# Optimization experiments

Measured on AMD Instinct MI355X. Metric: run time of the kernel, lower is better.

## Reference

```python
import jax, jax.numpy as jnp
import numpy as np
import math

L, B, D, H = 2048, 4, 1024, 16
DK = D // H
DFF = 4 * D
EPS = 1e-5


def setup_inputs() -> dict:
    key = jax.random.key(0)
    ks = jax.random.split(key, 16)
    s = 1.0 / math.sqrt(D)
    sf = 1.0 / math.sqrt(DFF)
    return {
        "x": jax.random.normal(ks[0], (L, B, D), jnp.float32),
        "Wq": jax.random.normal(ks[1], (D, D), jnp.float32) * s,
        "bq": jnp.zeros((D,), jnp.float32),
        "Wk": jax.random.normal(ks[2], (D, D), jnp.float32) * s,
        "bk": jnp.zeros((D,), jnp.float32),
        "Wv": jax.random.normal(ks[3], (D, D), jnp.float32) * s,
        "bv": jnp.zeros((D,), jnp.float32),
        "Wo": jax.random.normal(ks[4], (D, D), jnp.float32) * s,
        "bo": jnp.zeros((D,), jnp.float32),
        "W1": jax.random.normal(ks[5], (D, DFF), jnp.float32) * s,
        "b1": jnp.zeros((DFF,), jnp.float32),
        "W2": jax.random.normal(ks[6], (DFF, D), jnp.float32) * sf,
        "b2": jnp.zeros((D,), jnp.float32),
        "g1": jnp.ones((D,), jnp.float32),
        "be1": jnp.zeros((D,), jnp.float32),
        "g2": jnp.ones((D,), jnp.float32),
        "be2": jnp.zeros((D,), jnp.float32),
    }


def _layer_norm(x, g, b):
    mu = jnp.mean(x, axis=-1, keepdims=True)
    var = jnp.var(x, axis=-1, keepdims=True)
    return (x - mu) * jax.lax.rsqrt(var + EPS) * g + b


def reference(x, Wq, bq, Wk, bk, Wv, bv, Wo, bo, W1, b1, W2, b2, g1, be1, g2, be2):
    # x: (L, B, D)
    q = x @ Wq + bq
    k = x @ Wk + bk
    v = x @ Wv + bv
    # (L,B,H,dk) -> (B,H,L,dk)
    q = q.reshape(L, B, H, DK).transpose(1, 2, 0, 3)
    k = k.reshape(L, B, H, DK).transpose(1, 2, 0, 3)
    v = v.reshape(L, B, H, DK).transpose(1, 2, 0, 3)
    scale = 1.0 / math.sqrt(DK)
    scores = jnp.einsum('bhqd,bhkd->bhqk', q, k) * scale
    w = jax.nn.softmax(scores, axis=-1)
    attn = jnp.einsum('bhqk,bhkd->bhqd', w, v)  # (B,H,L,dk)
    attn = attn.transpose(2, 0, 1, 3).reshape(L, B, D)
    attn_out = attn @ Wo + bo
    x = _layer_norm(x + attn_out, g1, be1)
    h = jax.nn.gelu(x @ W1 + b1, approximate=False)
    ff = h @ W2 + b2
    return _layer_norm(x + ff, g2, be2)
```

## Files before the change

### kernel.cpp

```cpp
#include <hip/hip_runtime.h>

#define L_   2048
#define B_   4
#define D_   1024
#define H_   16
#define DK_  64
#define DFF_ 4096
#define NT_  (L_*B_)

typedef unsigned short u16;
typedef unsigned int   u32;
typedef __bf16 bf16x8 __attribute__((ext_vector_type(8)));
typedef float  f32x4  __attribute__((ext_vector_type(4)));

__device__ __forceinline__ u16 f2bf(float f) {
  u32 u = __float_as_uint(f);
  u += 0x7fffu + ((u >> 16) & 1u);
  return (u16)(u >> 16);
}
__device__ __forceinline__ float bf2f(u32 lo16) {
  return __uint_as_float(lo16 << 16);
}

#define GLDS16(g, l) __builtin_amdgcn_global_load_lds( \
    (const __attribute__((address_space(1))) void*)(g), \
    (__attribute__((address_space(3))) void*)(l), 16, 0, 0)

#define SCQ_ 0.18033688011112042f

__global__ __launch_bounds__(256) void transpose_w_k(
    const float* __restrict__ W, u16* __restrict__ Wt, int K, int N)
{
  __shared__ float tile[32][33];
  int n0 = blockIdx.x * 32, k0 = blockIdx.y * 32;
  int tx = threadIdx.x, ty = threadIdx.y;
#pragma unroll
  for (int i = ty; i < 32; i += 8)
    tile[i][tx] = W[(size_t)(k0 + i) * N + n0 + tx];
  __syncthreads();
#pragma unroll
  for (int i = ty; i < 32; i += 8)
    Wt[(size_t)(n0 + i) * K + k0 + tx] = f2bf(tile[tx][i]);
}

__global__ __launch_bounds__(256) void transpose_w4_k(
    const float* __restrict__ W0, const float* __restrict__ W1,
    const float* __restrict__ W2, const float* __restrict__ W3,
    u16* __restrict__ dst)
{
  __shared__ float tile[32][33];
  int z = blockIdx.z;
  const float* W = (z == 0) ? W0 : (z == 1) ? W1 : (z == 2) ? W2 : W3;
  u16* Wt = dst + (size_t)z * 1048576;
  int n0 = blockIdx.x * 32, k0 = blockIdx.y * 32;
  int tx = threadIdx.x, ty = threadIdx.y;
#pragma unroll
  for (int i = ty; i < 32; i += 8)
    tile[i][tx] = W[(size_t)(k0 + i) * 1024 + n0 + tx];
  __syncthreads();
#pragma unroll
  for (int i = ty; i < 32; i += 8)
    Wt[(size_t)(n0 + i) * 1024 + k0 + tx] = f2bf(tile[tx][i]);
}

__global__ __launch_bounds__(256) void f32_to_bf16_k(
    const float* __restrict__ in, u16* __restrict__ out, int n4)
{
  int i = blockIdx.x * 256 + threadIdx.x;
  if (i >= n4) return;
  float4 v = ((const float4*)in)[i];
  uint2 r;
  r.x = (u32)f2bf(v.x) | ((u32)f2bf(v.y) << 16);
  r.y = (u32)f2bf(v.z) | ((u32)f2bf(v.w) << 16);
  ((uint2*)out)[i] = r;
}

__global__ __launch_bounds__(256) void bias_concat_k(
    const float* __restrict__ bq, const float* __restrict__ bk,
    const float* __restrict__ bv, float* __restrict__ o)
{
  int i = blockIdx.x * 256 + threadIdx.x;
  float v = (i < 1024) ? bq[i] : ((i < 2048) ? bk[i - 1024] : bv[i - 2048]);
  o[i] = v;
}

template<int BN, int EPI>
__global__ __launch_bounds__(512, 2)
void gemm_pipe(const u16* __restrict__ A, const u16* __restrict__ Bt,
               const float* __restrict__ bias, const void* __restrict__ res,
               u16* __restrict__ outb, int M, int N, int K)
{
  constexpr int BM = 256;
  constexpr int NI  = 2 + BN / 128;
  constexpr int NWN = BN / 64;
  constexpr int NWM = 8 / NWN;
  constexpr int MIT = (BM / NWM) / 16;
  constexpr int NPH = MIT / 4;
  constexpr int BUFB = (BM + BN) * 64;
  __shared__ char SM[4 * BUFB];

  const int tid = threadIdx.x;
  const int w = tid >> 6, lane = tid & 63;
  const int l15 = lane & 15, l4 = lane >> 4;
  const int NK = K >> 5;

  const int gx = gridDim.x;
  int nwg = gx * gridDim.y;
  int id = blockIdx.y * gx + blockIdx.x;
  int q = nwg >> 3, r = nwg & 7;
  int xcd = id & 7, idx = id >> 3;
  int wg = (xcd < r ? xcd * (q + 1) : r * (q + 1) + (xcd - r) * q) + idx;
  const int m0 = (wg / gx) * BM, n0 = (wg % gx) * BN;
  const int wm = (w / NWN) * (BM / NWM), wn = (w % NWN) * 64;

  const u16* gsrc[NI];
#pragma unroll
  for (int k = 0; k < NI; ++k) {
    int o = k * 8192 + tid * 16;
    int col8 = (((o >> 4) ^ (o >> 6)) & 3);
    if (o < BM * 64) {
      int rrow = o >> 6;
      gsrc[k] = A + (size_t)(m0 + rrow) * K + col8 * 8;
    } else {
      int br = (o - BM * 64) >> 6;
      gsrc[k] = Bt + (size_t)(n0 + br) * K + col8 * 8;
    }
  }

  auto stage = [&](int t3, int k) {
    const u16* s = (t3 < NK) ? gsrc[k] + (size_t)t3 * 32 : gsrc[k];
    GLDS16(s, SM + (t3 & 3) * BUFB + k * 8192 + w * 1024);
  };

  for (int t3 = 0; t3 < 3; ++t3)
#pragma unroll
    for (int k = 0; k < NI; ++k) stage(t3, k);
  if constexpr (BN == 256) asm volatile("s_waitcnt vmcnt(8)" ::: "memory");
  else                     asm volatile("s_waitcnt vmcnt(6)" ::: "memory");
  asm volatile("s_barrier" ::: "memory");

  f32x4 acc[MIT][4];
#pragma unroll
  for (int i = 0; i < MIT; ++i)
#pragma unroll
    for (int j = 0; j < 4; ++j) acc[i][j] = (f32x4){0.f, 0.f, 0.f, 0.f};

  const int csw = (l4 ^ (l15 & 3)) * 16;

  for (int t = 0; t < NK; ++t) {
    const char* rb = SM + (t & 3) * BUFB;
    bf16x8 bfr[4];
#pragma unroll
    for (int ph = 0; ph < NPH; ++ph) {
      bf16x8 af[4];
#pragma unroll
      for (int mi = 0; mi < 4; ++mi)
        af[mi] = *(const bf16x8*)(rb + (wm + ph * 64 + mi * 16 + l15) * 64 + csw);
      if (ph == 0) {
#pragma unroll
        for (int nj = 0; nj < 4; ++nj)
          bfr[nj] = *(const bf16x8*)(rb + BM * 64 + (wn + nj * 16 + l15) * 64 + csw);
      }
      if constexpr (NPH == 2) {
        stage(t + 3, ph * 2 + 0);
        stage(t + 3, ph * 2 + 1);
      } else {
        stage(t + 3, 0); stage(t + 3, 1); stage(t + 3, 2);
      }
      asm volatile("s_barrier" ::: "memory");
      __builtin_amdgcn_s_setprio(1);
#pragma unroll
      for (int mi = 0; mi < 4; ++mi)
#pragma unroll
        for (int nj = 0; nj < 4; ++nj)
          acc[ph * 4 + mi][nj] = __builtin_amdgcn_mfma_f32_16x16x32_bf16(
              af[mi], bfr[nj], acc[ph * 4 + mi][nj], 0, 0, 0);
      __builtin_amdgcn_s_setprio(0);
      if (ph == NPH - 1) {
        if constexpr (BN == 256) asm volatile("s_waitcnt vmcnt(8)" ::: "memory");
        else                     asm volatile("s_waitcnt vmcnt(6)" ::: "memory");
      }
      asm volatile("s_barrier" ::: "memory");
    }
  }
  asm volatile("s_waitcnt vmcnt(0)" ::: "memory");

  const int gm = m0 + wm + l4 * 4;
  const int gn = n0 + wn + l15;
#pragma unroll
  for (int mi = 0; mi < MIT; ++mi) {
#pragma unroll
    for (int nj = 0; nj < 4; ++nj) {
      int col = gn + nj * 16;
      float bv = bias[col];
#pragma unroll
      for (int rr = 0; rr < 4; ++rr) {
        int row = gm + mi * 16 + rr;
        float v = acc[mi][nj][rr] + bv;
        if (EPI == 2) {
          float gv = 0.5f * v * (1.f + erff(v * 0.70710678118654752f));
          outb[(size_t)row * N + col] = f2bf(gv);
        } else if (EPI == 3) {
          int which = col >> 10, c1 = col & 1023;
          int ll = row >> 2, bb = row & 3;
          int hh = c1 >> 6, dd = c1 & 63;
          if (which == 0) v *= SCQ_;
          outb[(size_t)which * 8388608 +
               ((((size_t)(bb * H_ + hh)) * L_ + ll) << 6) + dd] = f2bf(v);
        } else if (EPI == 5) {
          size_t idxo = (size_t)row * N + col;
          outb[idxo] = f2bf(v + ((const float*)res)[idxo]);
        } else {
          size_t idxo = (size_t)row * N + col;
          outb[idxo] = f2bf(v + bf2f(((const u16*)res)[idxo]));
        }
      }
    }
  }
}

__global__ __launch_bounds__(256, 3)
void attn_fwd2(const u16* __restrict__ qp, const u16* __restrict__ kp,
               const u16* __restrict__ vp, u16* __restrict__ op)
{
  __shared__ u16 Ks[64 * 64];
  __shared__ u16 Vt[64 * 64];
  const int tid = threadIdx.x, w = tid >> 6, lane = tid & 63;
  const int l15 = lane & 15, l4 = lane >> 4;
  const int n = blockIdx.x;
  const int bh = (n & 7) | ((n >> 7) << 3);
  const int qi = (n >> 3) & 15;
  const int q0 = qi * 128;
  const u16* qb = qp + (size_t)bh * L_ * DK_;
  const u16* kb = kp + (size_t)bh * L_ * DK_;
  const u16* vb = vp + (size_t)bh * L_ * DK_;

  bf16x8 qf[2][2];
#pragma unroll
  for (int g = 0; g < 2; ++g)
#pragma unroll
    for (int kk = 0; kk < 2; ++kk)
      qf[g][kk] = *(const bf16x8*)&qb[(size_t)(q0 + g * 64 + w * 16 + l15) * DK_ +
                                      kk * 32 + l4 * 8];

  f32x4 accO[2][4];
#pragma unroll
  for (int g = 0; g < 2; ++g)
#pragma unroll
    for (int i = 0; i < 4; ++i) accO[g][i] = (f32x4){0.f, 0.f, 0.f, 0.f};
  float mrun[2] = {-1e30f, -1e30f}, lsum[2] = {0.f, 0.f};

  int rho0 = tid >> 3, rho1 = (256 + tid) >> 3, cseg = lane & 7;
  int kv0 = (rho0 & 32) | ((rho0 & 12) << 1) | ((rho0 & 16) >> 2) | (rho0 & 3);
  int kv1 = (rho1 & 32) | ((rho1 & 12) << 1) | ((rho1 & 16) >> 2) | (rho1 & 3);
  const u16* ksrc0 = kb + (size_t)kv0 * DK_ + ((cseg ^ (rho0 & 7)) << 3);
  const u16* ksrc1 = kb + (size_t)kv1 * DK_ + ((cseg ^ (rho1 & 7)) << 3);
  u16* kdst0 = &Ks[(w * 64) * 8];
  u16* kdst1 = &Ks[(256 + w * 64) * 8];

  const int vseg = tid & 7, vkvp = tid >> 3;
  const u16* vsrc = vb + (size_t)(vkvp * 2) * DK_ + vseg * 8;
  u32* vdst[8];
#pragma unroll
  for (int dd2 = 0; dd2 < 4; ++dd2) {
    int d0 = vseg * 8 + dd2 * 2, d1 = d0 + 1;
    vdst[dd2 * 2] = (u32*)((char*)Vt + d0 * 128 +
        ((((vkvp >> 2) ^ (d0 & 7) ^ (d0 >> 3)) << 4) | ((vkvp & 3) << 2)));
    vdst[dd2 * 2 + 1] = (u32*)((char*)Vt + d1 * 128 +
        ((((vkvp >> 2) ^ (d1 & 7) ^ (d1 >> 3)) << 4) | ((vkvp & 3) << 2)));
  }

  auto softmax_pack = [&](f32x4 (&s)[4], float& mr, float& ls,
                          f32x4 (&aO)[4], u32 (&pk)[2][4]) {
    float pm = fmaxf(fmaxf(s[0][0], s[0][1]), s[0][2]);
    pm = fmaxf(fmaxf(pm, s[0][3]), s[1][0]);
    pm = fmaxf(fmaxf(pm, s[1][1]), s[1][2]);
    pm = fmaxf(fmaxf(pm, s[1][3]), s[2][0]);
    pm = fmaxf(fmaxf(pm, s[2][1]), s[2][2]);
    pm = fmaxf(fmaxf(pm, s[2][3]), s[3][0]);
    pm = fmaxf(fmaxf(pm, s[3][1]), s[3][2]);
    pm = fmaxf(pm, s[3][3]);
    pm = fmaxf(pm, __shfl_xor(pm, 16));
    pm = fmaxf(pm, __shfl_xor(pm, 32));
    if (!__all(pm - mr <= 8.f)) {
      float mn = fmaxf(mr, pm);
      float alpha = exp2f(mr - mn);
      mr = mn;
      ls *= alpha;
#pragma unroll
      for (int rr = 0; rr < 4; ++rr) {
        float a4 = __shfl(alpha, l4 * 4 + rr);
        aO[0][rr] *= a4; aO[1][rr] *= a4; aO[2][rr] *= a4; aO[3][rr] *= a4;
      }
    }
#pragma unroll
    for (int i = 0; i < 4; ++i)
#pragma unroll
      for (int rr = 0; rr < 4; ++rr) s[i][rr] = exp2f(s[i][rr] - mr);
    float ps = 0.f;
#pragma unroll
    for (int i = 0; i < 4; ++i)
      ps += (s[i][0] + s[i][1]) + (s[i][2] + s[i][3]);
    ps += __shfl_xor(ps, 16);
    ps += __shfl_xor(ps, 32);
    ls += ps;
#pragma unroll
    for (int kk = 0; kk < 2; ++kk)
#pragma unroll
      for (int j2 = 0; j2 < 4; ++j2) {
        int nb = kk * 2 + (j2 >> 1);
        int rr = (j2 & 1) * 2;
        u32 rres;
        asm("v_cvt_pk_bf16_f32 %0, %1, %2" : "=v"(rres)
            : "v"(s[nb][rr]), "v"(s[nb][rr + 1]));
        pk[kk][j2] = rres;
      }
  };

  for (int t0 = 0; t0 < L_; t0 += 64) {
    __syncthreads();
    GLDS16(ksrc0 + (size_t)t0 * DK_, kdst0);
    GLDS16(ksrc1 + (size_t)t0 * DK_, kdst1);
    {
      const u16* src = vsrc + (size_t)t0 * DK_;
      uint4 a = *(const uint4*)src;
      uint4 b = *(const uint4*)(src + DK_);
#pragma unroll
      for (int dd2 = 0; dd2 < 4; ++dd2) {
        u32 ai = ((const u32*)&a)[dd2], bi = ((const u32*)&b)[dd2];
        *vdst[dd2 * 2]     = __builtin_amdgcn_perm(bi, ai, 0x05040100u);
        *vdst[dd2 * 2 + 1] = __builtin_amdgcn_perm(bi, ai, 0x07060302u);
      }
    }
    __syncthreads();

    f32x4 s0[4], s1[4];
#pragma unroll
    for (int i = 0; i < 4; ++i) {
      s0[i] = (f32x4){0.f, 0.f, 0.f, 0.f};
      s1[i] = (f32x4){0.f, 0.f, 0.f, 0.f};
    }
#pragma unroll
    for (int kk = 0; kk < 2; ++kk) {
#pragma unroll
      for (int nb = 0; nb < 4; ++nb) {
        int row = nb * 16 + l15;
        bf16x8 kf = *(const bf16x8*)((const char*)Ks + row * 128 +
                                     (((kk * 4 + l4) ^ (row & 7)) << 4));
        s0[nb] = __builtin_amdgcn_mfma_f32_16x16x32_bf16(kf, qf[0][kk], s0[nb], 0, 0, 0);
        s1[nb] = __builtin_amdgcn_mfma_f32_16x16x32_bf16(kf, qf[1][kk], s1[nb], 0, 0, 0);
      }
    }

    u32 pk0[2][4], pk1[2][4];
    softmax_pack(s0, mrun[0], lsum[0], accO[0], pk0);
    softmax_pack(s1, mrun[1], lsum[1], accO[1], pk1);

#pragma unroll
    for (int kk = 0; kk < 2; ++kk) {
      bf16x8 pa0, pa1;
      ((u32*)&pa0)[0] = pk0[kk][0]; ((u32*)&pa0)[1] = pk0[kk][1];
      ((u32*)&pa0)[2] = pk0[kk][2]; ((u32*)&pa0)[3] = pk0[kk][3];
      ((u32*)&pa1)[0] = pk1[kk][0]; ((u32*)&pa1)[1] = pk1[kk][1];
      ((u32*)&pa1)[2] = pk1[kk][2]; ((u32*)&pa1)[3] = pk1[kk][3];
#pragma unroll
      for (int nb2 = 0; nb2 < 4; ++nb2) {
        int drow = nb2 * 16 + l15;
        bf16x8 vf = *(const bf16x8*)((const char*)Vt + drow * 128 +
                                     (((kk * 4 + l4) ^ (drow & 7) ^ (drow >> 3)) << 4));
        accO[0][nb2] = __builtin_amdgcn_mfma_f32_16x16x32_bf16(pa0, vf, accO[0][nb2], 0, 0, 0);
        accO[1][nb2] = __builtin_amdgcn_mfma_f32_16x16x32_bf16(pa1, vf, accO[1][nb2], 0, 0, 0);
      }
    }
  }

  const int bb = bh >> 4, hh = bh & 15;
#pragma unroll
  for (int g = 0; g < 2; ++g) {
    float invl = 1.f / lsum[g];
#pragma unroll
    for (int rr = 0; rr < 4; ++rr) {
      float rl = __shfl(invl, l4 * 4 + rr);
      int qg = q0 + g * 64 + w * 16 + l4 * 4 + rr;
      size_t base = ((size_t)qg * B_ + bb) * D_ + hh * 64;
#pragma unroll
      for (int nb2 = 0; nb2 < 4; ++nb2)
        op[base + nb2 * 16 + l15] = f2bf(accO[g][nb2][rr] * rl);
    }
  }
}

__global__ __launch_bounds__(256) void layernorm_bf_k(
    const u16* __restrict__ y, const float* __restrict__ g, const float* __restrict__ be,
    float* __restrict__ of, u16* __restrict__ ob)
{
  int row = blockIdx.x, tid = threadIdx.x;
  uint2 raw = *(const uint2*)&y[(size_t)row * D_ + tid * 4];
  float v0 = bf2f(raw.x & 0xffffu), v1 = bf2f(raw.x >> 16);
  float v2 = bf2f(raw.y & 0xffffu), v3 = bf2f(raw.y >> 16);
  float s = (v0 + v1) + (v2 + v3);
  float ss = v0 * v0 + v1 * v1 + v2 * v2 + v3 * v3;
#pragma unroll
  for (int msk = 32; msk >= 1; msk >>= 1) {
    s += __shfl_xor(s, msk);
    ss += __shfl_xor(ss, msk);
  }
  __shared__ float rs[4], rss[4];
  if ((tid & 63) == 0) { rs[tid >> 6] = s; rss[tid >> 6] = ss; }
  __syncthreads();
  s = rs[0] + rs[1] + rs[2] + rs[3];
  ss = rss[0] + rss[1] + rss[2] + rss[3];
  float mu = s * (1.f / D_);
  float var = ss * (1.f / D_) - mu * mu;
  float rstd = rsqrtf(var + 1e-5f);
  int c = tid * 4;
  float o0 = (v0 - mu) * rstd * g[c + 0] + be[c + 0];
  float o1 = (v1 - mu) * rstd * g[c + 1] + be[c + 1];
  float o2 = (v2 - mu) * rstd * g[c + 2] + be[c + 2];
  float o3 = (v3 - mu) * rstd * g[c + 3] + be[c + 3];
  if (of) {
    float4 o = {o0, o1, o2, o3};
    *(float4*)&of[(size_t)row * D_ + c] = o;
  }
  if (ob) {
    uint2 r;
    r.x = (u32)f2bf(o0) | ((u32)f2bf(o1) << 16);
    r.y = (u32)f2bf(o2) | ((u32)f2bf(o3) << 16);
    *(uint2*)&ob[(size_t)row * D_ + c] = r;
  }
}

extern "C" void kernel_launch(void* const* d_in, const int* in_sizes, int n_in,
                              void* d_out, int out_size, void* d_ws, size_t ws_size,
                              hipStream_t stream)
{
  const float* x   = (const float*)d_in[0];
  const float* Wq  = (const float*)d_in[1];
  const float* bq  = (const float*)d_in[2];
  const float* Wk  = (const float*)d_in[3];
  const float* bk  = (const float*)d_in[4];
  const float* Wv  = (const float*)d_in[5];
  const float* bv  = (const float*)d_in[6];
  const float* Wo  = (const float*)d_in[7];
  const float* bo  = (const float*)d_in[8];
  const float* W1f = (const float*)d_in[9];
  const float* b1  = (const float*)d_in[10];
  const float* W2f = (const float*)d_in[11];
  const float* b2  = (const float*)d_in[12];
  const float* g1  = (const float*)d_in[13];
  const float* be1 = (const float*)d_in[14];
  const float* g2  = (const float*)d_in[15];
  const float* be2 = (const float*)d_in[16];

  char* ws = (char*)d_ws;
  const size_t MB = 1024 * 1024;
  u16* WqT  = (u16*)(ws + 0 * MB);
  u16* WoT  = (u16*)(ws + 6 * MB);
  u16* W1T  = (u16*)(ws + 8 * MB);
  u16* W2T  = (u16*)(ws + 16 * MB);
  u16* xb   = (u16*)(ws + 24 * MB);
  u16* qp   = (u16*)(ws + 40 * MB);
  u16* astd = (u16*)(ws + 88 * MB);
  u16* yb   = (u16*)(ws + 104 * MB);
  u16* x1b  = (u16*)(ws + 120 * MB);
  u16* hbuf = (u16*)(ws + 136 * MB);
  float* bcat = (float*)(ws + 200 * MB);
  u16* kp = qp + 8388608;
  u16* vp = qp + 16777216;

  dim3 tb(32, 8);
  transpose_w4_k<<<dim3(32, 32, 4), tb, 0, stream>>>(Wq, Wk, Wv, Wo, WqT);
  transpose_w_k<<<dim3(128, 32), tb, 0, stream>>>(W1f, W1T, D_, DFF_);
  transpose_w_k<<<dim3(32, 128), tb, 0, stream>>>(W2f, W2T, DFF_, D_);
  f32_to_bf16_k<<<NT_ * D_ / 4 / 256, 256, 0, stream>>>(x, xb, NT_ * D_ / 4);
  bias_concat_k<<<12, 256, 0, stream>>>(bq, bk, bv, bcat);

  gemm_pipe<128, 3><<<dim3(24, 32), 512, 0, stream>>>(
      xb, WqT, bcat, nullptr, qp, NT_, 3072, D_);

  attn_fwd2<<<1024, 256, 0, stream>>>(qp, kp, vp, astd);

  gemm_pipe<128, 5><<<dim3(8, 32), 512, 0, stream>>>(
      astd, WoT, bo, x, yb, NT_, D_, D_);
  layernorm_bf_k<<<NT_, 256, 0, stream>>>(yb, g1, be1, nullptr, x1b);
  gemm_pipe<256, 2><<<dim3(16, 32), 512, 0, stream>>>(
      x1b, W1T, b1, nullptr, hbuf, NT_, DFF_, D_);
  gemm_pipe<128, 6><<<dim3(8, 32), 512, 0, stream>>>(
      hbuf, W2T, b2, x1b, yb, NT_, D_, DFF_);
  layernorm_bf_k<<<NT_, 256, 0, stream>>>(yb, g2, be2, (float*)d_out, nullptr);
}
```

Measured before the change: 494.4 us.

## Double-buffer K/V tiles in attention kernel to overlap loads with MFMA

Attention kernel now keeps two LDS buffers for K and transposed V and prefetches the next tile (K via global-to-LDS loads, V via register loads packed into LDS after softmax) while computing on the current one. This drops one of the two barriers per iteration and hides global load latency behind compute. LDS use doubles to 32KB per block, which may reduce occupancy at launch bound 3 blocks/CU.

```diff
diff --git a/kernel.cpp b/kernel.cpp
--- a/kernel.cpp
+++ b/kernel.cpp
@@ -223,8 +223,8 @@
 void attn_fwd2(const u16* __restrict__ qp, const u16* __restrict__ kp,
                const u16* __restrict__ vp, u16* __restrict__ op)
 {
-  __shared__ u16 Ks[64 * 64];
-  __shared__ u16 Vt[64 * 64];
+  __shared__ u16 Ks[2][64 * 64];
+  __shared__ u16 Vt[2][64 * 64];
   const int tid = threadIdx.x, w = tid >> 6, lane = tid & 63;
   const int l15 = lane & 15, l4 = lane >> 4;
   const int n = blockIdx.x;
@@ -255,20 +255,27 @@
   int kv1 = (rho1 & 32) | ((rho1 & 12) << 1) | ((rho1 & 16) >> 2) | (rho1 & 3);
   const u16* ksrc0 = kb + (size_t)kv0 * DK_ + ((cseg ^ (rho0 & 7)) << 3);
   const u16* ksrc1 = kb + (size_t)kv1 * DK_ + ((cseg ^ (rho1 & 7)) << 3);
-  u16* kdst0 = &Ks[(w * 64) * 8];
-  u16* kdst1 = &Ks[(256 + w * 64) * 8];
 
   const int vseg = tid & 7, vkvp = tid >> 3;
   const u16* vsrc = vb + (size_t)(vkvp * 2) * DK_ + vseg * 8;
-  u32* vdst[8];
+  u32 voff[8];
 #pragma unroll
   for (int dd2 = 0; dd2 < 4; ++dd2) {
     int d0 = vseg * 8 + dd2 * 2, d1 = d0 + 1;
-    vdst[dd2 * 2] = (u32*)((char*)Vt + d0 * 128 +
-        ((((vkvp >> 2) ^ (d0 & 7) ^ (d0 >> 3)) << 4) | ((vkvp & 3) << 2)));
-    vdst[dd2 * 2 + 1] = (u32*)((char*)Vt + d1 * 128 +
-        ((((vkvp >> 2) ^ (d1 & 7) ^ (d1 >> 3)) << 4) | ((vkvp & 3) << 2)));
-  }
+    voff[dd2 * 2] = d0 * 128 +
+        ((((vkvp >> 2) ^ (d0 & 7) ^ (d0 >> 3)) << 4) | ((vkvp & 3) << 2));
+    voff[dd2 * 2 + 1] = d1 * 128 +
+        ((((vkvp >> 2) ^ (d1 & 7) ^ (d1 >> 3)) << 4) | ((vkvp & 3) << 2));
+  }
+
+  auto packV = [&](int buf, uint4 a, uint4 b) {
+#pragma unroll
+    for (int dd2 = 0; dd2 < 4; ++dd2) {
+      u32 ai = ((const u32*)&a)[dd2], bi = ((const u32*)&b)[dd2];
+      *(u32*)((char*)Vt[buf] + voff[dd2 * 2])     = __builtin_amdgcn_perm(bi, ai, 0x05040100u);
+      *(u32*)((char*)Vt[buf] + voff[dd2 * 2 + 1]) = __builtin_amdgcn_perm(bi, ai, 0x07060302u);
+    }
+  };
 
   auto softmax_pack = [&](f32x4 (&s)[4], float& mr, float& ls,
                           f32x4 (&aO)[4], u32 (&pk)[2][4]) {
@@ -317,22 +324,27 @@
       }
   };
 
-  for (int t0 = 0; t0 < L_; t0 += 64) {
-    __syncthreads();
-    GLDS16(ksrc0 + (size_t)t0 * DK_, kdst0);
-    GLDS16(ksrc1 + (size_t)t0 * DK_, kdst1);
-    {
-      const u16* src = vsrc + (size_t)t0 * DK_;
-      uint4 a = *(const uint4*)src;
-      uint4 b = *(const uint4*)(src + DK_);
-#pragma unroll
-      for (int dd2 = 0; dd2 < 4; ++dd2) {
-        u32 ai = ((const u32*)&a)[dd2], bi = ((const u32*)&b)[dd2];
-        *vdst[dd2 * 2]     = __builtin_amdgcn_perm(bi, ai, 0x05040100u);
-        *vdst[dd2 * 2 + 1] = __builtin_amdgcn_perm(bi, ai, 0x07060302u);
-      }
-    }
-    __syncthreads();
+  {
+    uint4 a = *(const uint4*)vsrc;
+    uint4 b = *(const uint4*)(vsrc + DK_);
+    GLDS16(ksrc0, &Ks[0][w * 512]);
+    GLDS16(ksrc1, &Ks[0][2048 + w * 512]);
+    packV(0, a, b);
+  }
+  __syncthreads();
+
+  constexpr int NTI = L_ / 64;
+  for (int t = 0; t < NTI; ++t) {
+    const int cur = t & 1;
+    const bool pf = (t + 1 < NTI);
+    const int tn = pf ? t + 1 : t;
+
+    uint4 va = *(const uint4*)(vsrc + (size_t)(tn * 64) * DK_);
+    uint4 vbv = *(const uint4*)(vsrc + (size_t)(tn * 64) * DK_ + DK_);
+    if (pf) {
+      GLDS16(ksrc0 + (size_t)((t + 1) * 64) * DK_, &Ks[cur ^ 1][w * 512]);
+      GLDS16(ksrc1 + (size_t)((t + 1) * 64) * DK_, &Ks[cur ^ 1][2048 + w * 512]);
+    }
 
     f32x4 s0[4], s1[4];
 #pragma unroll
@@ -345,7 +357,7 @@
 #pragma unroll
       for (int nb = 0; nb < 4; ++nb) {
         int row = nb * 16 + l15;
-        bf16x8 kf = *(const bf16x8*)((const char*)Ks + row * 128 +
+        bf16x8 kf = *(const bf16x8*)((const char*)Ks[cur] + row * 128 +
                                      (((kk * 4 + l4) ^ (row & 7)) << 4));
         s0[nb] = __builtin_amdgcn_mfma_f32_16x16x32_bf16(kf, qf[0][kk], s0[nb], 0, 0, 0);
         s1[nb] = __builtin_amdgcn_mfma_f32_16x16x32_bf16(kf, qf[1][kk], s1[nb], 0, 0, 0);
@@ -355,6 +367,8 @@
     u32 pk0[2][4], pk1[2][4];
     softmax_pack(s0, mrun[0], lsum[0], accO[0], pk0);
     softmax_pack(s1, mrun[1], lsum[1], accO[1], pk1);
+
+    if (pf) packV(cur ^ 1, va, vbv);
 
 #pragma unroll
     for (int kk = 0; kk < 2; ++kk) {
@@ -366,12 +380,13 @@
 #pragma unroll
       for (int nb2 = 0; nb2 < 4; ++nb2) {
         int drow = nb2 * 16 + l15;
-        bf16x8 vf = *(const bf16x8*)((const char*)Vt + drow * 128 +
+        bf16x8 vf = *(const bf16x8*)((const char*)Vt[cur] + drow * 128 +
                                      (((kk * 4 + l4) ^ (drow & 7) ^ (drow >> 3)) << 4));
         accO[0][nb2] = __builtin_amdgcn_mfma_f32_16x16x32_bf16(pa0, vf, accO[0][nb2], 0, 0, 0);
         accO[1][nb2] = __builtin_amdgcn_mfma_f32_16x16x32_bf16(pa1, vf, accO[1][nb2], 0, 0, 0);
       }
     }
+    __syncthreads();
   }
 
   const int bb = bh >> 4, hh = bh & 15;
```

After: 490.8 us. Within noise of the previous version (-0.7%).
